# Kernel tuning notes

Measured on AMD Instinct MI355X. Metric: run time of the kernel, lower is better.

Reference implementation:

```python
import jax, jax.numpy as jnp
import numpy as np

D = 200            # embedding_dim == GRU hidden size
N_LABELS = 28000   # MeSH label count (graph nodes)
VOCAB = 50000
B = 4
T_AB = 384         # abstract length
T_TI = 64          # title length
N_EDGES = 224000   # ~8 edges per label node


def reverse_padded(x, lengths):
    # reverse the first lengths[b] timesteps of each padded sequence
    T = x.shape[1]
    t = jnp.arange(T)
    idx = jnp.where(t[None, :] < lengths[:, None], lengths[:, None] - 1 - t[None, :], t[None, :])
    return jnp.take_along_axis(x, idx[:, :, None], axis=1)


def gru_dir(x, lengths, wih, whh, bih, bhh, reverse):
    # PyTorch-semantics GRU over a padded batch (packed-sequence equivalent):
    # hidden state freezes past each sequence length; padded outputs are zero.
    Bb, T, _ = x.shape
    Hh = whh.shape[1]
    if reverse:
        x = reverse_padded(x, lengths)
    gx = jnp.einsum('bti,gi->btg', x, wih) + bih   # [B,T,3H], torch gate order r,z,n

    def step(h, inp):
        g_t, t = inp
        gh = h @ whh.T + bhh
        r = jax.nn.sigmoid(g_t[:, :Hh] + gh[:, :Hh])
        z = jax.nn.sigmoid(g_t[:, Hh:2 * Hh] + gh[:, Hh:2 * Hh])
        n = jnp.tanh(g_t[:, 2 * Hh:] + r * gh[:, 2 * Hh:])
        h_new = (1.0 - z) * n + z * h
        mask = (t < lengths)[:, None]
        h = jnp.where(mask, h_new, h)
        return h, jnp.where(mask, h_new, 0.0)

    h0 = jnp.zeros((Bb, Hh), x.dtype)
    _, outs = jax.lax.scan(step, h0, (jnp.swapaxes(gx, 0, 1), jnp.arange(T)))
    outs = jnp.swapaxes(outs, 0, 1)
    if reverse:
        outs = reverse_padded(outs, lengths)
    return outs


def forward_impl(input_abstract, input_title, ab_length, title_length, edge_src, edge_dst,
                 g_node_feature, emb,
                 wih_l0f, whh_l0f, bih_l0f, bhh_l0f, wih_l0b, whh_l0b, bih_l0b, bhh_l0b,
                 wih_l1f, whh_l1f, bih_l1f, bhh_l1f, wih_l1b, whh_l1b, bih_l1b, bhh_l1b,
                 gcn_w1, gcn_b1, gcn_w2, gcn_b2, fc1_w, fc1_b, fc2_w, fc2_b):
    # --- LabelNet: two GCN layers (copy_src message + sum reduce, then Linear) ---
    def gcn_layer(feat, W, b):
        agg = jax.ops.segment_sum(feat[edge_src], edge_dst, num_segments=N_LABELS)
        return agg @ W.T + b

    h = jax.nn.relu(gcn_layer(g_node_feature, gcn_w1, gcn_b1))
    lab = gcn_layer(h, gcn_w2, gcn_b2)
    label_feature = jnp.concatenate([lab, g_node_feature], axis=1)   # [N, 2D]

    gru_params = [
        (wih_l0f, whh_l0f, bih_l0f, bhh_l0f, wih_l0b, whh_l0b, bih_l0b, bhh_l0b),
        (wih_l1f, whh_l1f, bih_l1f, bhh_l1f, wih_l1b, whh_l1b, bih_l1b, bhh_l1b),
    ]

    def branch(tokens, lengths):
        x = emb[tokens]                                              # [B,T,D]
        for (wif, whf, bif, bhf, wib, whb, bib, bhb) in gru_params:
            f = gru_dir(x, lengths, wif, whf, bif, bhf, False)
            bwd = gru_dir(x, lengths, wib, whb, bib, bhb, True)
            x = jnp.concatenate([f, bwd], axis=-1)                   # [B,T,2D]
        # doc-label cross attention: softmax over the sequence dim (dim=1).
        # Padded positions output zero vectors -> logit 0, included in softmax
        # exactly as in the original torch code.
        atten = jax.nn.softmax(jnp.einsum('btd,nd->btn', x, label_feature), axis=1)
        return jnp.einsum('btd,btn->bnd', x, atten)                  # [B,N,2D]

    feat = branch(input_title, title_length) + branch(input_abstract, ab_length)
    y = jax.nn.leaky_relu(feat @ fc1_w.T + fc1_b, negative_slope=0.2)
    y = jax.nn.leaky_relu(y @ fc2_w.T + fc2_b, negative_slope=0.2)
    return y[..., 0]                                                 # [B, N]


def setup_inputs():
    key = jax.random.key(0)
    ks = jax.random.split(key, 32)
    it = iter(range(32))
    def nk():
        return ks[next(it)]
    s = 0.05
    inp = {}
    inp['input_abstract'] = jax.random.randint(nk(), (B, T_AB), 0, VOCAB)
    inp['input_title'] = jax.random.randint(nk(), (B, T_TI), 0, VOCAB)
    inp['ab_length'] = jax.random.randint(nk(), (B,), T_AB // 2, T_AB + 1).at[0].set(T_AB)
    inp['title_length'] = jax.random.randint(nk(), (B,), T_TI // 2, T_TI + 1).at[0].set(T_TI)
    inp['edge_src'] = jax.random.randint(nk(), (N_EDGES,), 0, N_LABELS)
    inp['edge_dst'] = jax.random.randint(nk(), (N_EDGES,), 0, N_LABELS)
    inp['g_node_feature'] = jax.random.normal(nk(), (N_LABELS, D)) * s
    inp['emb'] = jax.random.normal(nk(), (VOCAB, D)) * s
    for l in range(2):
        in_dim = D if l == 0 else 2 * D
        for d in ('f', 'b'):
            inp['wih_l%d%s' % (l, d)] = jax.random.normal(nk(), (3 * D, in_dim)) * s
            inp['whh_l%d%s' % (l, d)] = jax.random.normal(nk(), (3 * D, D)) * s
            inp['bih_l%d%s' % (l, d)] = jnp.zeros((3 * D,))
            inp['bhh_l%d%s' % (l, d)] = jnp.zeros((3 * D,))
    inp['gcn_w1'] = jax.random.normal(nk(), (D, D)) * s
    inp['gcn_b1'] = jnp.zeros((D,))
    inp['gcn_w2'] = jax.random.normal(nk(), (D, D)) * s
    inp['gcn_b2'] = jnp.zeros((D,))
    inp['fc1_w'] = jax.random.normal(nk(), (D, 2 * D)) * s
    inp['fc1_b'] = jnp.zeros((D,))
    inp['fc2_w'] = jax.random.normal(nk(), (1, D)) * s
    inp['fc2_b'] = jnp.zeros((1,))
    return inp


def reference(input_abstract, input_title, ab_length, title_length, edge_src, edge_dst,
              g_node_feature, emb,
              wih_l0f, whh_l0f, bih_l0f, bhh_l0f, wih_l0b, whh_l0b, bih_l0b, bhh_l0b,
              wih_l1f, whh_l1f, bih_l1f, bhh_l1f, wih_l1b, whh_l1b, bih_l1b, bhh_l1b,
              gcn_w1, gcn_b1, gcn_w2, gcn_b2, fc1_w, fc1_b, fc2_w, fc2_b):
    return forward_impl(input_abstract, input_title, ab_length, title_length, edge_src, edge_dst,
                        g_node_feature, emb,
                        wih_l0f, whh_l0f, bih_l0f, bhh_l0f, wih_l0b, whh_l0b, bih_l0b, bhh_l0b,
                        wih_l1f, whh_l1f, bih_l1f, bhh_l1f, wih_l1b, whh_l1b, bih_l1b, bhh_l1b,
                        gcn_w1, gcn_b1, gcn_w2, gcn_b2, fc1_w, fc1_b, fc2_w, fc2_b)
```

## Files before the change

kernel.cpp:

```cpp
#include <hip/hip_runtime.h>
#include <math.h>

#define NLAB 28000
#define NEDGE 224000
#define XFS 224

typedef _Float16 f16;
typedef _Float16 f16x8 __attribute__((ext_vector_type(8)));
typedef float f32x4 __attribute__((ext_vector_type(4)));


__device__ __forceinline__ void atomAddF(float* p, float v) {
  unsafeAtomicAdd(p, v);
}

struct RecurArgs {
  const float* gx[4];
  const float* wF[4];
  const float* bh[4];
  float* out[4];
  const int* len[4];
  int Tl[4];
  int dir[4];
};

#define COMPB(V, B) ((B) == 0 ? (V).x : (B) == 1 ? (V).y : (B) == 2 ? (V).z : (V).w)


__global__ void embed_gather(const int* __restrict__ tok, const float* __restrict__ emb,
                             float* __restrict__ x, int rows) {
  int idx = blockIdx.x * blockDim.x + threadIdx.x;
  if (idx >= rows * 50) return;
  int r = idx / 50, c = idx - r * 50;
  *(float4*)&x[(size_t)r * 200 + c * 4] =
      *(const float4*)&emb[(size_t)tok[r] * 200 + c * 4];
}


__global__ void pack_whhF(const float* __restrict__ whh, f16* __restrict__ out) {
  int e = blockIdx.x * 256 + threadIdx.x;
  if (e >= 40 * 7 * 512) return;
  int frag = e >> 9, r = e & 511;
  int l = r >> 3, j = r & 7;
  int mt = frag / 7, kt = frag - mt * 7;
  int m = mt * 16 + (l & 15);
  int k = kt * 32 + ((l >> 4) << 2) + (j & 3) + ((j >> 2) << 4);
  float v = (m < 600 && k < 200) ? whh[(size_t)m * 200 + k] : 0.f;
  f16 hi = (f16)v;
  out[e] = hi;
  out[40 * 7 * 512 + e] = (f16)((v - (float)hi) * 2048.f);
}


template <int RELU, int BIAS>
__global__ __launch_bounds__(256, 2) void gemm_nt(
    const float* __restrict__ A, const float* __restrict__ Wt,
    const float* __restrict__ bias, float* __restrict__ C,
    int M, int N, int K, int ldc) {
  __shared__ float As[16][68];
  __shared__ float Bs[16][68];
  int tx = threadIdx.x & 15, ty = threadIdx.x >> 4;
  int m0 = blockIdx.y * 64, n0 = blockIdx.x * 64;
  float c[4][4] = {};
  int row = threadIdx.x >> 2;
  int kk = (threadIdx.x & 3) * 4;
  for (int k0 = 0; k0 < K; k0 += 16) {
    int gk = k0 + kk;
    float a0 = 0, a1 = 0, a2 = 0, a3 = 0;
    float b0 = 0, b1 = 0, b2 = 0, b3 = 0;
    int gm = m0 + row;
    if (gm < M) {
      if (gk + 3 < K) {
        float4 v = *(const float4*)&A[(size_t)gm * K + gk];
        a0 = v.x; a1 = v.y; a2 = v.z; a3 = v.w;
      } else {
        if (gk + 0 < K) a0 = A[(size_t)gm * K + gk + 0];
        if (gk + 1 < K) a1 = A[(size_t)gm * K + gk + 1];
        if (gk + 2 < K) a2 = A[(size_t)gm * K + gk + 2];
        if (gk + 3 < K) a3 = A[(size_t)gm * K + gk + 3];
      }
    }
    int gn = n0 + row;
    if (gn < N) {
      if (gk + 3 < K) {
        float4 v = *(const float4*)&Wt[(size_t)gn * K + gk];
        b0 = v.x; b1 = v.y; b2 = v.z; b3 = v.w;
      } else {
        if (gk + 0 < K) b0 = Wt[(size_t)gn * K + gk + 0];
        if (gk + 1 < K) b1 = Wt[(size_t)gn * K + gk + 1];
        if (gk + 2 < K) b2 = Wt[(size_t)gn * K + gk + 2];
        if (gk + 3 < K) b3 = Wt[(size_t)gn * K + gk + 3];
      }
    }
    As[kk + 0][row] = a0; As[kk + 1][row] = a1; As[kk + 2][row] = a2; As[kk + 3][row] = a3;
    Bs[kk + 0][row] = b0; Bs[kk + 1][row] = b1; Bs[kk + 2][row] = b2; Bs[kk + 3][row] = b3;
    __syncthreads();
#pragma unroll
    for (int k = 0; k < 16; k++) {
      float4 a4 = *(const float4*)&As[k][ty * 4];
      float4 b4 = *(const float4*)&Bs[k][tx * 4];
      c[0][0] = fmaf(a4.x, b4.x, c[0][0]); c[0][1] = fmaf(a4.x, b4.y, c[0][1]);
      c[0][2] = fmaf(a4.x, b4.z, c[0][2]); c[0][3] = fmaf(a4.x, b4.w, c[0][3]);
      c[1][0] = fmaf(a4.y, b4.x, c[1][0]); c[1][1] = fmaf(a4.y, b4.y, c[1][1]);
      c[1][2] = fmaf(a4.y, b4.z, c[1][2]); c[1][3] = fmaf(a4.y, b4.w, c[1][3]);
      c[2][0] = fmaf(a4.z, b4.x, c[2][0]); c[2][1] = fmaf(a4.z, b4.y, c[2][1]);
      c[2][2] = fmaf(a4.z, b4.z, c[2][2]); c[2][3] = fmaf(a4.z, b4.w, c[2][3]);
      c[3][0] = fmaf(a4.w, b4.x, c[3][0]); c[3][1] = fmaf(a4.w, b4.y, c[3][1]);
      c[3][2] = fmaf(a4.w, b4.z, c[3][2]); c[3][3] = fmaf(a4.w, b4.w, c[3][3]);
    }
    __syncthreads();
  }
#pragma unroll
  for (int i = 0; i < 4; i++) {
    int gm = m0 + ty * 4 + i;
    if (gm >= M) continue;
#pragma unroll
    for (int j = 0; j < 4; j++) {
      int gn = n0 + tx * 4 + j;
      if (gn >= N) continue;
      float v = c[i][j];
      if (BIAS) v += bias[gn];
      if (RELU) v = fmaxf(v, 0.f);
      C[(size_t)gm * ldc + gn] = v;
    }
  }
}


__global__ __launch_bounds__(512, 1) void gru_fused(RecurArgs a,
    const float* __restrict__ gfeat, const int* __restrict__ esrc,
    const int* __restrict__ edst, float* __restrict__ gagg) {
  __shared__ __align__(16) f16 wlds[16][7][512];
  __shared__ __align__(16) f16 hfrag[2][7][512];
  __shared__ float h[200][4];
  __shared__ float gh[600][4];
  __shared__ float bhs[600];
  __shared__ int lens[4];

  if (blockIdx.x >= 4) {
    int lane = threadIdx.x & 63;
    if (lane >= 50) return;
    int nb = gridDim.x - 4;
    int wav = (blockIdx.x - 4) * 8 + (threadIdx.x >> 6);
    for (int e = wav; e < NEDGE; e += nb * 8) {
      int s = esrc[e], d = edst[e];
      float4 v = *(const float4*)&gfeat[(size_t)s * 200 + lane * 4];
      float* p = &gagg[(size_t)d * 200 + lane * 4];
      atomAddF(p + 0, v.x); atomAddF(p + 1, v.y);
      atomAddF(p + 2, v.z); atomAddF(p + 3, v.w);
    }
    return;
  }

  int blk = blockIdx.x;
  const float* __restrict__ gx = a.gx[blk];
  const f16* __restrict__ whiP = (const f16*)a.wF[blk];
  const float* __restrict__ bh = a.bh[blk];
  float* __restrict__ outp = a.out[blk];
  const int* lenp = a.len[blk];
  int TT = a.Tl[blk];
  int bwd = a.dir[blk];
  int dirOff = bwd ? 200 : 0;

  int tid = threadIdx.x, lane = tid & 63, w = tid >> 6;
  int l15 = lane & 15, lg = lane >> 4;

  for (int i = tid; i < 800; i += 512) ((float*)h)[i] = 0.f;
  for (int i = tid; i < 600; i += 512) bhs[i] = bh[i];
  for (int i = tid; i < 2 * 7 * 512; i += 512) ((f16*)hfrag)[i] = (f16)0.f;
  if (tid < 4) lens[tid] = lenp[tid];

#pragma unroll
  for (int i = 0; i < 2; i++)
#pragma unroll
    for (int kt = 0; kt < 7; kt++)
      *(f16x8*)&wlds[w * 2 + i][kt][lane * 8] =
          *(const f16x8*)(whiP + ((size_t)((w * 5 + i) * 7 + kt)) * 512 + lane * 8);
  __syncthreads();
  int maxlen = max(max(lens[0], lens[1]), max(lens[2], lens[3]));

  for (int s = 0; s < maxlen; s++) {
    float pgx[3][4];
    if (tid < 200) {
#pragma unroll
      for (int b = 0; b < 4; b++) {
        int Lb = lens[b];
        if (s < Lb) {
          int ta = bwd ? (Lb - 1 - s) : s;
          const float* gxr = gx + (size_t)(b * TT + ta) * 600;
          pgx[0][b] = gxr[tid];
          pgx[1][b] = gxr[200 + tid];
          pgx[2][b] = gxr[400 + tid];
        }
      }
    }
    f32x4 acc1[5], acc2[5];
#pragma unroll
    for (int i = 0; i < 5; i++) {
      acc1[i] = (f32x4){0.f, 0.f, 0.f, 0.f};
      acc2[i] = (f32x4){0.f, 0.f, 0.f, 0.f};
    }
#pragma unroll
    for (int kt = 0; kt < 7; kt++) {
      f16x8 hhi = *(const f16x8*)&hfrag[0][kt][lane * 8];
      f16x8 hlo = *(const f16x8*)&hfrag[1][kt][lane * 8];
#pragma unroll
      for (int i = 0; i < 5; i++) {
        const f16* base = whiP + ((size_t)((w * 5 + i) * 7 + kt)) * 512 + lane * 8;
        f16x8 whi = (i < 2) ? *(const f16x8*)&wlds[w * 2 + i][kt][lane * 8]
                            : *(const f16x8*)base;
        f16x8 wlo = *(const f16x8*)(base + (size_t)40 * 7 * 512);
        acc1[i] = __builtin_amdgcn_mfma_f32_16x16x32_f16(whi, hhi, acc1[i], 0, 0, 0);
        acc2[i] = __builtin_amdgcn_mfma_f32_16x16x32_f16(wlo, hhi, acc2[i], 0, 0, 0);
        acc2[i] = __builtin_amdgcn_mfma_f32_16x16x32_f16(whi, hlo, acc2[i], 0, 0, 0);
      }
    }
    if (l15 < 4) {
#pragma unroll
      for (int i = 0; i < 5; i++) {
        int mbase = (w * 5 + i) * 16 + lg * 4;
#pragma unroll
        for (int r = 0; r < 4; r++) {
          int m = mbase + r;
          if (m < 600) gh[m][l15] = acc1[i][r] + acc2[i][r] * (1.f / 2048.f);
        }
      }
    }
    __syncthreads();
    if (tid < 200) {
      int u = tid;
      float4 hold = *(const float4*)&h[u][0];
      float4 hnew = hold;
      float br = bhs[u], bz = bhs[200 + u], bn = bhs[400 + u];
#pragma unroll
      for (int b = 0; b < 4; b++) {
        int Lb = lens[b];
        if (s < Lb) {
          int ta = bwd ? (Lb - 1 - s) : s;
          float r = 1.f / (1.f + expf(-(pgx[0][b] + gh[u][b] + br)));
          float z = 1.f / (1.f + expf(-(pgx[1][b] + gh[200 + u][b] + bz)));
          float n = tanhf(pgx[2][b] + r * (gh[400 + u][b] + bn));
          float hn = (1.f - z) * n + z * COMPB(hold, b);
          if (b == 0) hnew.x = hn; else if (b == 1) hnew.y = hn;
          else if (b == 2) hnew.z = hn; else hnew.w = hn;
          outp[(size_t)(b * TT + ta) * 400 + dirOff + u] = hn;
        }
      }
      *(float4*)&h[u][0] = hnew;
      int kt = u >> 5;
      int lbase = ((u >> 2) & 3) << 4;
      int j = (u & 3) | (((u >> 4) & 1) << 2);
#pragma unroll
      for (int b = 0; b < 4; b++) {
        float hv = COMPB(hnew, b);
        f16 hi = (f16)hv;
        f16 lo = (f16)((hv - (float)hi) * 2048.f);
        hfrag[0][kt][(lbase + b) * 8 + j] = hi;
        hfrag[1][kt][(lbase + b) * 8 + j] = lo;
      }
    }
    __syncthreads();
  }
}


__global__ void cvt_lf_frags(const float* __restrict__ lab, const float* __restrict__ gnf,
                             f16* __restrict__ out) {
  int e = blockIdx.x * 256 + threadIdx.x;
  if (e >= 1752 * 13 * 512) return;
  int frag = e >> 9, r = e & 511;
  int l = r >> 3, j = r & 7;
  int nsub = frag / 13, kt = frag - nsub * 13;
  int label = nsub * 16 + (l & 15);
  int k = kt * 32 + ((l >> 4) << 2) + (j & 3) + ((j >> 2) << 4);
  float v = 0.f;
  if (label < NLAB && k < 400)
    v = (k < 200) ? lab[(size_t)label * 200 + k] : gnf[(size_t)label * 200 + k - 200];
  out[e] = (f16)v;
}

__global__ void cvt_x_frags(const float* __restrict__ x, f16* __restrict__ out, int TT) {
  int e = blockIdx.x * 256 + threadIdx.x;
  if (e >= 4 * TT * 13 * 512) return;
  int frag = e >> 9, r = e & 511;
  int l = r >> 3, j = r & 7;
  int kt = frag % 13, bt = frag / 13;
  int tt = bt % TT, b = bt / TT;
  int t = tt * 16 + (l & 15);
  int k = kt * 32 + ((l >> 4) << 2) + (j & 3) + ((j >> 2) << 4);
  float v = (k < 400) ? x[((size_t)b * TT * 16 + t) * 400 + k] : 0.f;
  out[e] = (f16)v;
}

__global__ void cvt_v_frags(const float* __restrict__ xf, f16* __restrict__ out, int KT) {
  int e = blockIdx.x * 256 + threadIdx.x;
  if (e >= 4 * KT * 13 * 2 * 512) return;
  int idx = e >> 9, r = e & 511;
  int l = r >> 3, j = r & 7;
  int hl = idx & 1, rest = idx >> 1;
  int dt = rest % 13, rest2 = rest / 13;
  int kt = rest2 % KT, b = rest2 / KT;
  int t = kt * 32 + ((l >> 4) << 2) + (j & 3) + ((j >> 2) << 4);
  int d = dt * 16 + (l & 15);
  float v = xf[((size_t)b * KT * 32 + t) * XFS + d];
  float hi = (float)(f16)v;
  out[e] = hl ? (f16)((v - hi) * 2048.f) : (f16)v;
}


__global__ __launch_bounds__(256, 2) void attn_mfma(
    const f16* __restrict__ lfF, const f16* __restrict__ xFab, const f16* __restrict__ xFti,
    const f16* __restrict__ vFab, const f16* __restrict__ vFti,
    const float* __restrict__ fc1b, const float* __restrict__ fc2w,
    const float* __restrict__ fc2b, float* __restrict__ outp) {
  __shared__ float SB[2][32][65];
  __shared__ float CRS[2][2][16];
  __shared__ float LIS[2][2][16];

  int tid = threadIdx.x, lane = tid & 63, w = tid >> 6;
  int nh = w >> 1, hl = w & 1;
  int b = blockIdx.y, nt = blockIdx.x;
  int l15 = lane & 15, lg = lane >> 4;

  f32x4 acc[2][13];
#pragma unroll
  for (int ns = 0; ns < 2; ns++)
#pragma unroll
    for (int dt = 0; dt < 13; dt++) acc[ns][dt] = (f32x4){0.f, 0.f, 0.f, 0.f};
  float mrun[4] = {-INFINITY, -INFINITY, -INFINITY, -INFINITY};
  float lrun[4] = {0.f, 0.f, 0.f, 0.f};

  for (int c = 0; c < 7; c++) {
    const bool ti = (c == 6);
    const f16* xb = ti ? xFti + (size_t)b * (4 * 13 * 512)
                       : xFab + ((size_t)(b * 24 + c * 4)) * 13 * 512;
    f32x4 S[2][2];
#pragma unroll
    for (int ns = 0; ns < 2; ns++)
#pragma unroll
      for (int ts = 0; ts < 2; ts++) S[ns][ts] = (f32x4){0.f, 0.f, 0.f, 0.f};
#pragma unroll
    for (int kh = 0; kh < 2; kh++) {
      const int kt0 = kh ? 7 : 0;
      const int ktn = kh ? 6 : 7;
      f16x8 la[2][7];
#pragma unroll
      for (int ns = 0; ns < 2; ns++) {
        const f16* lp = lfF + (((size_t)(nt * 4 + nh * 2 + ns)) * 13 + kt0) * 512 + lane * 8;
#pragma unroll
        for (int k = 0; k < 7; k++)
          if (k < ktn) la[ns][k] = *(const f16x8*)(lp + (size_t)k * 512);
      }
#pragma unroll
      for (int ts = 0; ts < 2; ts++) {
        const f16* xp = xb + (((size_t)(hl * 2 + ts)) * 13 + kt0) * 512 + lane * 8;
        f16x8 xa[7];
#pragma unroll
        for (int k = 0; k < 7; k++)
          if (k < ktn) xa[k] = *(const f16x8*)(xp + (size_t)k * 512);
#pragma unroll
        for (int ns = 0; ns < 2; ns++)
#pragma unroll
          for (int k = 0; k < 7; k++)
            if (k < ktn)
              S[ns][ts] = __builtin_amdgcn_mfma_f32_16x16x32_f16(la[ns][k], xa[k], S[ns][ts], 0, 0, 0);
      }
    }
    __syncthreads();
#pragma unroll
    for (int ns = 0; ns < 2; ns++)
#pragma unroll
      for (int ts = 0; ts < 2; ts++)
#pragma unroll
        for (int r = 0; r < 4; r++)
          SB[nh][ns * 16 + lg * 4 + r][(hl * 2 + ts) * 16 + l15] = S[ns][ts][r];
    __syncthreads();
    {
      float vv[4][4];
#pragma unroll
      for (int r = 0; r < 4; r++)
#pragma unroll
        for (int ts = 0; ts < 4; ts++)
          vv[r][ts] = SB[nh][hl * 16 + lg * 4 + r][ts * 16 + l15];
#pragma unroll
      for (int r = 0; r < 4; r++) {
        float tm = fmaxf(fmaxf(vv[r][0], vv[r][1]), fmaxf(vv[r][2], vv[r][3]));
        tm = fmaxf(tm, __shfl_xor(tm, 1));
        tm = fmaxf(tm, __shfl_xor(tm, 2));
        tm = fmaxf(tm, __shfl_xor(tm, 4));
        tm = fmaxf(tm, __shfl_xor(tm, 8));
        if (!ti) {
          float mn = fmaxf(mrun[r], tm);
          float cr = expf(mrun[r] - mn);
          float s = 0.f;
#pragma unroll
          for (int ts = 0; ts < 4; ts++) { vv[r][ts] = expf(vv[r][ts] - mn); s += vv[r][ts]; }
          s += __shfl_xor(s, 1); s += __shfl_xor(s, 2);
          s += __shfl_xor(s, 4); s += __shfl_xor(s, 8);
          lrun[r] = lrun[r] * cr + s;
          mrun[r] = mn;
#pragma unroll
          for (int ts = 0; ts < 4; ts++)
            SB[nh][hl * 16 + lg * 4 + r][ts * 16 + l15] = vv[r][ts];
          if (l15 == 0) {
            CRS[nh][hl][lg * 4 + r] = cr;
            if (c == 5) LIS[nh][hl][lg * 4 + r] = 1.f / lrun[r];
          }
        } else {
          float s = 0.f;
#pragma unroll
          for (int ts = 0; ts < 4; ts++) { vv[r][ts] = expf(vv[r][ts] - tm); s += vv[r][ts]; }
          s += __shfl_xor(s, 1); s += __shfl_xor(s, 2);
          s += __shfl_xor(s, 4); s += __shfl_xor(s, 8);
          float inv = 1.f / s;
#pragma unroll
          for (int ts = 0; ts < 4; ts++)
            SB[nh][hl * 16 + lg * 4 + r][ts * 16 + l15] = vv[r][ts] * inv;
        }
      }
    }
    __syncthreads();
    if (!ti) {
#pragma unroll
      for (int ns = 0; ns < 2; ns++)
#pragma unroll
        for (int r = 0; r < 4; r++) {
          float cr = CRS[nh][ns][lg * 4 + r];
#pragma unroll
          for (int dt = 0; dt < 13; dt++) acc[ns][dt][r] *= cr;
        }
    } else {
#pragma unroll
      for (int ns = 0; ns < 2; ns++)
#pragma unroll
        for (int r = 0; r < 4; r++) {
          float li = LIS[nh][ns][lg * 4 + r];
#pragma unroll
          for (int dt = 0; dt < 13; dt++) acc[ns][dt][r] *= li;
        }
    }
    f16x8 pf[2][2];
#pragma unroll
    for (int ns = 0; ns < 2; ns++)
#pragma unroll
      for (int kt = 0; kt < 2; kt++)
#pragma unroll
        for (int j = 0; j < 8; j++) {
          int col = kt * 32 + (lg << 2) + (j & 3) + ((j >> 2) << 4);
          pf[ns][kt][j] = (f16)SB[nh][ns * 16 + l15][col];
        }
#pragma unroll
    for (int dt = 0; dt < 13; dt++)
#pragma unroll
      for (int kt = 0; kt < 2; kt++) {
        const f16* vp = (ti ? vFti + (((size_t)((b * 2 + kt) * 13 + dt)) * 2 + hl) * 512
                            : vFab + (((size_t)((b * 12 + c * 2 + kt) * 13 + dt)) * 2 + hl) * 512)
                        + lane * 8;
        f16x8 vf = *(const f16x8*)vp;
#pragma unroll
        for (int ns = 0; ns < 2; ns++)
          acc[ns][dt] = __builtin_amdgcn_mfma_f32_16x16x32_f16(pf[ns][kt], vf, acc[ns][dt], 0, 0, 0);
      }
  }

  float part[2][4] = {{0.f, 0.f, 0.f, 0.f}, {0.f, 0.f, 0.f, 0.f}};
#pragma unroll
  for (int p = 0; p < 4; p++) {
    const int dt0 = p * 4;
    const int dtn = (p == 3) ? 1 : 4;
    __syncthreads();
    if (hl) {
#pragma unroll
      for (int ns = 0; ns < 2; ns++)
#pragma unroll
        for (int q = 0; q < 4; q++)
          if (q < dtn)
#pragma unroll
            for (int r = 0; r < 4; r++)
              SB[nh][ns * 16 + lg * 4 + r][q * 16 + l15] = acc[ns][dt0 + q][r];
    }
    __syncthreads();
    if (!hl) {
#pragma unroll
      for (int ns = 0; ns < 2; ns++)
#pragma unroll
        for (int q = 0; q < 4; q++)
          if (q < dtn)
#pragma unroll
            for (int r = 0; r < 4; r++) {
              int d = (dt0 + q) * 16 + l15;
              float y = acc[ns][dt0 + q][r] +
                        SB[nh][ns * 16 + lg * 4 + r][q * 16 + l15] * (1.f / 2048.f);
              if (d < 200) {
                y += fc1b[d];
                y = y >= 0.f ? y : 0.2f * y;
                part[ns][r] = fmaf(y, fc2w[d], part[ns][r]);
              }
            }
    }
  }
  if (!hl) {
#pragma unroll
    for (int ns = 0; ns < 2; ns++)
#pragma unroll
      for (int r = 0; r < 4; r++) {
        float s = part[ns][r];
        s += __shfl_xor(s, 1); s += __shfl_xor(s, 2);
        s += __shfl_xor(s, 4); s += __shfl_xor(s, 8);
        part[ns][r] = s;
      }
    if (l15 == 0) {
      float f2b = fc2b[0];
#pragma unroll
      for (int ns = 0; ns < 2; ns++)
#pragma unroll
        for (int r = 0; r < 4; r++) {
          int label = nt * 64 + nh * 32 + ns * 16 + lg * 4 + r;
          if (label < NLAB) {
            float y = part[ns][r] + f2b;
            y = y >= 0.f ? y : 0.2f * y;
            outp[(size_t)b * NLAB + label] = y;
          }
        }
    }
  }
}


extern "C" void kernel_launch(void* const* d_in, const int* in_sizes, int n_in,
                              void* d_out, int out_size, void* d_ws, size_t ws_size,
                              hipStream_t stream) {
  (void)in_sizes; (void)n_in; (void)out_size; (void)ws_size;
  const int* tok_ab = (const int*)d_in[0];
  const int* tok_ti = (const int*)d_in[1];
  const int* len_ab = (const int*)d_in[2];
  const int* len_ti = (const int*)d_in[3];
  const int* esrc = (const int*)d_in[4];
  const int* edst = (const int*)d_in[5];
  const float* gnf = (const float*)d_in[6];
  const float* emb = (const float*)d_in[7];
  const float* wih0f = (const float*)d_in[8],  *whh0f = (const float*)d_in[9];
  const float* bih0f = (const float*)d_in[10], *bhh0f = (const float*)d_in[11];
  const float* wih0b = (const float*)d_in[12], *whh0b = (const float*)d_in[13];
  const float* bih0b = (const float*)d_in[14], *bhh0b = (const float*)d_in[15];
  const float* wih1f = (const float*)d_in[16], *whh1f = (const float*)d_in[17];
  const float* bih1f = (const float*)d_in[18], *bhh1f = (const float*)d_in[19];
  const float* wih1b = (const float*)d_in[20], *whh1b = (const float*)d_in[21];
  const float* bih1b = (const float*)d_in[22], *bhh1b = (const float*)d_in[23];
  const float* gw1 = (const float*)d_in[24], *gb1 = (const float*)d_in[25];
  const float* gw2 = (const float*)d_in[26], *gb2 = (const float*)d_in[27];
  const float* fc1w = (const float*)d_in[28], *fc1b = (const float*)d_in[29];
  const float* fc2w = (const float*)d_in[30], *fc2b = (const float*)d_in[31];

  float* W = (float*)d_ws;
  float* agg  = W;
  f16*   lfF  = (f16*)W;
  float* hbuf = W + 5830656;
  float* lab  = W + 5830656;
  float* x0ab   = W + 11200000;
  float* x0ti   = W + 11507200;
  float* whhF0f = W + 11558400;
  float* whhF0b = W + 11701760;
  float* whhF1f = W + 11845120;
  float* whhF1b = W + 11988480;
  float* gxfab  = W + 12131840;
  float* gxbab  = W + 13053440;
  float* gxfti  = W + 13975040;
  float* gxbti  = W + 14128640;
  float* out0ab = W + 14282240;
  float* out0ti = W + 14896640;
  float* out1ab = W + 14999040;
  float* out1ti = W + 15613440;
  float* xf1ab  = W + 15715840;
  float* xf1ti  = W + 16059904;
  f16* xFab = (f16*)(W + 12131840);
  f16* xFti = (f16*)(W + 12451328);
  f16* vFab = (f16*)(W + 12504576);
  f16* vFti = (f16*)(W + 12824064);

  dim3 gGcn(4, 438);
  dim3 gGxAb(10, 24), gGxTi(10, 4);
  int packN = (40 * 7 * 512 + 255) / 256;

  embed_gather<<<(1536 * 50 + 255) / 256, 256, 0, stream>>>(tok_ab, emb, x0ab, 1536);
  embed_gather<<<(256 * 50 + 255) / 256, 256, 0, stream>>>(tok_ti, emb, x0ti, 256);
  pack_whhF<<<packN, 256, 0, stream>>>(whh0f, (f16*)whhF0f);
  pack_whhF<<<packN, 256, 0, stream>>>(whh0b, (f16*)whhF0b);
  pack_whhF<<<packN, 256, 0, stream>>>(whh1f, (f16*)whhF1f);
  pack_whhF<<<packN, 256, 0, stream>>>(whh1b, (f16*)whhF1b);
  hipMemsetAsync(out0ab, 0, (size_t)1835008 * sizeof(float), stream);

  gemm_nt<0, 1><<<gGxAb, 256, 0, stream>>>(x0ab, wih0f, bih0f, gxfab, 1536, 600, 200, 600);
  gemm_nt<0, 1><<<gGxAb, 256, 0, stream>>>(x0ab, wih0b, bih0b, gxbab, 1536, 600, 200, 600);
  gemm_nt<0, 1><<<gGxTi, 256, 0, stream>>>(x0ti, wih0f, bih0f, gxfti, 256, 600, 200, 600);
  gemm_nt<0, 1><<<gGxTi, 256, 0, stream>>>(x0ti, wih0b, bih0b, gxbti, 256, 600, 200, 600);
  hipMemsetAsync(agg, 0, 5600000 * sizeof(float), stream);

  RecurArgs r0;
  r0.gx[0] = gxfab; r0.gx[1] = gxbab; r0.gx[2] = gxfti; r0.gx[3] = gxbti;
  r0.wF[0] = whhF0f; r0.wF[1] = whhF0b; r0.wF[2] = whhF0f; r0.wF[3] = whhF0b;
  r0.bh[0] = bhh0f; r0.bh[1] = bhh0b; r0.bh[2] = bhh0f; r0.bh[3] = bhh0b;
  r0.out[0] = out0ab; r0.out[1] = out0ab; r0.out[2] = out0ti; r0.out[3] = out0ti;
  r0.len[0] = len_ab; r0.len[1] = len_ab; r0.len[2] = len_ti; r0.len[3] = len_ti;
  r0.Tl[0] = 384; r0.Tl[1] = 384; r0.Tl[2] = 64; r0.Tl[3] = 64;
  r0.dir[0] = 0; r0.dir[1] = 1; r0.dir[2] = 0; r0.dir[3] = 1;
  gru_fused<<<252, 512, 0, stream>>>(r0, gnf, esrc, edst, agg);

  gemm_nt<1, 1><<<gGcn, 256, 0, stream>>>(agg, gw1, gb1, hbuf, NLAB, 200, 200, 200);
  hipMemsetAsync(agg, 0, 5600000 * sizeof(float), stream);
  gemm_nt<0, 1><<<gGxAb, 256, 0, stream>>>(out0ab, wih1f, bih1f, gxfab, 1536, 600, 400, 600);
  gemm_nt<0, 1><<<gGxAb, 256, 0, stream>>>(out0ab, wih1b, bih1b, gxbab, 1536, 600, 400, 600);
  gemm_nt<0, 1><<<gGxTi, 256, 0, stream>>>(out0ti, wih1f, bih1f, gxfti, 256, 600, 400, 600);
  gemm_nt<0, 1><<<gGxTi, 256, 0, stream>>>(out0ti, wih1b, bih1b, gxbti, 256, 600, 400, 600);

  RecurArgs r1 = r0;
  r1.wF[0] = whhF1f; r1.wF[1] = whhF1b;
  r1.wF[2] = whhF1f; r1.wF[3] = whhF1b;
  r1.bh[0] = bhh1f; r1.bh[1] = bhh1b; r1.bh[2] = bhh1f; r1.bh[3] = bhh1b;
  r1.out[0] = out1ab; r1.out[1] = out1ab; r1.out[2] = out1ti; r1.out[3] = out1ti;
  gru_fused<<<252, 512, 0, stream>>>(r1, hbuf, esrc, edst, agg);

  gemm_nt<0, 1><<<gGcn, 256, 0, stream>>>(agg, gw2, gb2, lab, NLAB, 200, 200, 200);
  cvt_lf_frags<<<(1752 * 13 * 512 + 255) / 256, 256, 0, stream>>>(lab, gnf, lfF);

  gemm_nt<0, 0><<<dim3(4, 24), 256, 0, stream>>>(out1ab, fc1w, nullptr, xf1ab, 1536, 200, 400, XFS);
  gemm_nt<0, 0><<<dim3(4, 4), 256, 0, stream>>>(out1ti, fc1w, nullptr, xf1ti, 256, 200, 400, XFS);

  cvt_x_frags<<<(4 * 24 * 13 * 512 + 255) / 256, 256, 0, stream>>>(out1ab, xFab, 24);
  cvt_x_frags<<<(4 * 4 * 13 * 512 + 255) / 256, 256, 0, stream>>>(out1ti, xFti, 4);
  cvt_v_frags<<<(4 * 12 * 13 * 2 * 512 + 255) / 256, 256, 0, stream>>>(xf1ab, vFab, 12);
  cvt_v_frags<<<(4 * 2 * 13 * 2 * 512 + 255) / 256, 256, 0, stream>>>(xf1ti, vFti, 2);

  attn_mfma<<<dim3(438, 4), 256, 0, stream>>>(
      lfF, xFab, xFti, vFab, vFti, fc1b, fc2w, fc2b, (float*)d_out);
}
```

Measured before the change: 5.891 ms.

## Fuse GCN linear layer and label fragment conversion into GRU side blocks

The helper blocks of the persistent GRU kernel previously only scattered edge features with atomics. They now also wait on a grid-wide atomic counter barrier and then run the GCN linear layer (matvec per label row with bias and optional ReLU). In the second launch they pass a second barrier and convert the label features to f16 MFMA fragments. This removes three separate kernel launches and hides the GCN work behind the serial GRU recurrence. In exchange the grid shrinks from 252 to 132 blocks and the fused GEMM is a naive per-row FMA loop reading weights from global memory. The software grid barrier relies on all 132 blocks being resident at once.

```diff
diff --git a/kernel.cpp b/kernel.cpp
--- a/kernel.cpp
+++ b/kernel.cpp
@@ -129,7 +129,10 @@
 
 __global__ __launch_bounds__(512, 1) void gru_fused(RecurArgs a,
     const float* __restrict__ gfeat, const int* __restrict__ esrc,
-    const int* __restrict__ edst, float* __restrict__ gagg) {
+    const int* __restrict__ edst, float* __restrict__ gagg,
+    const float* __restrict__ gw, const float* __restrict__ gb,
+    float* __restrict__ gout, int relu, int doCvt,
+    const float* __restrict__ gnfp, f16* __restrict__ lfFp, int* __restrict__ cnt) {
   __shared__ __align__(16) f16 wlds[16][7][512];
   __shared__ __align__(16) f16 hfrag[2][7][512];
   __shared__ float h[200][4];
@@ -138,16 +141,59 @@
   __shared__ int lens[4];
 
   if (blockIdx.x >= 4) {
-    int lane = threadIdx.x & 63;
-    if (lane >= 50) return;
+    int tid = threadIdx.x;
+    int lane = tid & 63;
     int nb = gridDim.x - 4;
-    int wav = (blockIdx.x - 4) * 8 + (threadIdx.x >> 6);
-    for (int e = wav; e < NEDGE; e += nb * 8) {
-      int s = esrc[e], d = edst[e];
-      float4 v = *(const float4*)&gfeat[(size_t)s * 200 + lane * 4];
-      float* p = &gagg[(size_t)d * 200 + lane * 4];
-      atomAddF(p + 0, v.x); atomAddF(p + 1, v.y);
-      atomAddF(p + 2, v.z); atomAddF(p + 3, v.w);
+    if (lane < 50) {
+      int wav = (blockIdx.x - 4) * 8 + (tid >> 6);
+      for (int e = wav; e < NEDGE; e += nb * 8) {
+        int s = esrc[e], d = edst[e];
+        float4 v = *(const float4*)&gfeat[(size_t)s * 200 + lane * 4];
+        float* p = &gagg[(size_t)d * 200 + lane * 4];
+        atomAddF(p + 0, v.x); atomAddF(p + 1, v.y);
+        atomAddF(p + 2, v.z); atomAddF(p + 3, v.w);
+      }
+    }
+    __syncthreads();
+    if (tid == 0) {
+      __threadfence();
+      __hip_atomic_fetch_add(&cnt[0], 1, __ATOMIC_ACQ_REL, __HIP_MEMORY_SCOPE_AGENT);
+      while (__hip_atomic_load(&cnt[0], __ATOMIC_ACQUIRE, __HIP_MEMORY_SCOPE_AGENT) < nb) {}
+    }
+    __syncthreads();
+    float* arow = (float*)wlds;
+    for (int m = blockIdx.x - 4; m < NLAB; m += nb) {
+      __syncthreads();
+      for (int k = tid; k < 200; k += 512) arow[k] = gagg[(size_t)m * 200 + k];
+      __syncthreads();
+      if (tid < 200) {
+        float acc = gb[tid];
+        const float* wr = gw + (size_t)tid * 200;
+#pragma unroll 4
+        for (int k = 0; k < 200; k++) acc = fmaf(arow[k], wr[k], acc);
+        if (relu) acc = fmaxf(acc, 0.f);
+        gout[(size_t)m * 200 + tid] = acc;
+      }
+    }
+    if (doCvt) {
+      __syncthreads();
+      if (tid == 0) {
+        __threadfence();
+        __hip_atomic_fetch_add(&cnt[1], 1, __ATOMIC_ACQ_REL, __HIP_MEMORY_SCOPE_AGENT);
+        while (__hip_atomic_load(&cnt[1], __ATOMIC_ACQUIRE, __HIP_MEMORY_SCOPE_AGENT) < nb) {}
+      }
+      __syncthreads();
+      for (int e = (blockIdx.x - 4) * 512 + tid; e < 1752 * 13 * 512; e += nb * 512) {
+        int frag = e >> 9, r = e & 511;
+        int l = r >> 3, j = r & 7;
+        int nsub = frag / 13, kt = frag - nsub * 13;
+        int label = nsub * 16 + (l & 15);
+        int k = kt * 32 + ((l >> 4) << 2) + (j & 3) + ((j >> 2) << 4);
+        float v = 0.f;
+        if (label < NLAB && k < 400)
+          v = (k < 200) ? gout[(size_t)label * 200 + k] : gnfp[(size_t)label * 200 + k - 200];
+        lfFp[e] = (f16)v;
+      }
     }
     return;
   }
@@ -263,21 +309,6 @@
   }
 }
 
-
-__global__ void cvt_lf_frags(const float* __restrict__ lab, const float* __restrict__ gnf,
-                             f16* __restrict__ out) {
-  int e = blockIdx.x * 256 + threadIdx.x;
-  if (e >= 1752 * 13 * 512) return;
-  int frag = e >> 9, r = e & 511;
-  int l = r >> 3, j = r & 7;
-  int nsub = frag / 13, kt = frag - nsub * 13;
-  int label = nsub * 16 + (l & 15);
-  int k = kt * 32 + ((l >> 4) << 2) + (j & 3) + ((j >> 2) << 4);
-  float v = 0.f;
-  if (label < NLAB && k < 400)
-    v = (k < 200) ? lab[(size_t)label * 200 + k] : gnf[(size_t)label * 200 + k - 200];
-  out[e] = (f16)v;
-}
 
 __global__ void cvt_x_frags(const float* __restrict__ x, f16* __restrict__ out, int TT) {
   int e = blockIdx.x * 256 + threadIdx.x;
@@ -559,6 +590,7 @@
   float* lab  = W + 5830656;
   float* x0ab   = W + 11200000;
   float* x0ti   = W + 11507200;
+  int*   cnt    = (int*)(W + 11550000);
   float* whhF0f = W + 11558400;
   float* whhF0b = W + 11701760;
   float* whhF1f = W + 11845120;
@@ -578,7 +610,6 @@
   f16* vFab = (f16*)(W + 12504576);
   f16* vFti = (f16*)(W + 12824064);
 
-  dim3 gGcn(4, 438);
   dim3 gGxAb(10, 24), gGxTi(10, 4);
   int packN = (40 * 7 * 512 + 255) / 256;
 
@@ -595,6 +626,7 @@
   gemm_nt<0, 1><<<gGxTi, 256, 0, stream>>>(x0ti, wih0f, bih0f, gxfti, 256, 600, 200, 600);
   gemm_nt<0, 1><<<gGxTi, 256, 0, stream>>>(x0ti, wih0b, bih0b, gxbti, 256, 600, 200, 600);
   hipMemsetAsync(agg, 0, 5600000 * sizeof(float), stream);
+  hipMemsetAsync(cnt, 0, 2 * sizeof(int), stream);
 
   RecurArgs r0;
   r0.gx[0] = gxfab; r0.gx[1] = gxbab; r0.gx[2] = gxfti; r0.gx[3] = gxbti;
@@ -604,10 +636,11 @@
   r0.len[0] = len_ab; r0.len[1] = len_ab; r0.len[2] = len_ti; r0.len[3] = len_ti;
   r0.Tl[0] = 384; r0.Tl[1] = 384; r0.Tl[2] = 64; r0.Tl[3] = 64;
   r0.dir[0] = 0; r0.dir[1] = 1; r0.dir[2] = 0; r0.dir[3] = 1;
-  gru_fused<<<252, 512, 0, stream>>>(r0, gnf, esrc, edst, agg);
-
-  gemm_nt<1, 1><<<gGcn, 256, 0, stream>>>(agg, gw1, gb1, hbuf, NLAB, 200, 200, 200);
+  gru_fused<<<132, 512, 0, stream>>>(r0, gnf, esrc, edst, agg,
+                                     gw1, gb1, hbuf, 1, 0, gnf, lfF, cnt);
+
   hipMemsetAsync(agg, 0, 5600000 * sizeof(float), stream);
+  hipMemsetAsync(cnt, 0, 2 * sizeof(int), stream);
   gemm_nt<0, 1><<<gGxAb, 256, 0, stream>>>(out0ab, wih1f, bih1f, gxfab, 1536, 600, 400, 600);
   gemm_nt<0, 1><<<gGxAb, 256, 0, stream>>>(out0ab, wih1b, bih1b, gxbab, 1536, 600, 400, 600);
   gemm_nt<0, 1><<<gGxTi, 256, 0, stream>>>(out0ti, wih1f, bih1f, gxfti, 256, 600, 400, 600);
@@ -618,10 +651,8 @@
   r1.wF[2] = whhF1f; r1.wF[3] = whhF1b;
   r1.bh[0] = bhh1f; r1.bh[1] = bhh1b; r1.bh[2] = bhh1f; r1.bh[3] = bhh1b;
   r1.out[0] = out1ab; r1.out[1] = out1ab; r1.out[2] = out1ti; r1.out[3] = out1ti;
-  gru_fused<<<252, 512, 0, stream>>>(r1, hbuf, esrc, edst, agg);
-
-  gemm_nt<0, 1><<<gGcn, 256, 0, stream>>>(agg, gw2, gb2, lab, NLAB, 200, 200, 200);
-  cvt_lf_frags<<<(1752 * 13 * 512 + 255) / 256, 256, 0, stream>>>(lab, gnf, lfF);
+  gru_fused<<<132, 512, 0, stream>>>(r1, hbuf, esrc, edst, agg,
+                                     gw2, gb2, lab, 0, 1, gnf, lfF, cnt);
 
   gemm_nt<0, 0><<<dim3(4, 24), 256, 0, stream>>>(out1ab, fc1w, nullptr, xf1ab, 1536, 200, 400, XFS);
   gemm_nt<0, 0><<<dim3(4, 4), 256, 0, stream>>>(out1ti, fc1w, nullptr, xf1ti, 256, 200, 400, XFS);
```

Result: faster. 5.370 ms (median of 2 runs) (-8.9%).
